# Kernel tuning notes

Hardware: AMD Instinct MI355X
Metric: run time of the kernel (lower is better)

The kernel has to match this reference:

```python
import jax, jax.numpy as jnp
import numpy as np

N_GRAPHS = 20000
N_NODES = 7          # nodes per NAS cell
HID = 256            # hidden_dim
N_OPS = 5
TAU = 1.0


def _glorot(key, shape):
    s = 1.0 / np.sqrt(shape[0])
    return jax.random.normal(key, shape, jnp.float32) * s


def setup_inputs() -> dict:
    key = jax.random.key(0)
    ks = jax.random.split(key, 12)
    N = N_GRAPHS * N_NODES
    # fully-connected DAG edges inside each graph (upper triangular, 21 per graph)
    sl, dl = np.triu_indices(N_NODES, k=1)
    offs = (np.arange(N_GRAPHS) * N_NODES)[:, None]
    src = (offs + sl[None, :]).reshape(-1)
    dst = (offs + dl[None, :]).reshape(-1)
    edge_index = jnp.asarray(np.stack([src, dst]), dtype=jnp.int32)  # [2, E]
    batch = jnp.asarray(np.repeat(np.arange(N_GRAPHS), N_NODES), dtype=jnp.int32)
    E = edge_index.shape[1]
    return {
        "x": jax.random.normal(ks[0], (N, HID), jnp.float32),
        "edge_index": edge_index,
        "batch": batch,
        "W1": _glorot(ks[1], (HID, HID)), "b1": jnp.zeros((HID,), jnp.float32),
        "W2": _glorot(ks[2], (HID, HID)), "b2": jnp.zeros((HID,), jnp.float32),
        "We": _glorot(ks[3], (2 * HID, 2)), "be": jnp.zeros((2,), jnp.float32),
        "Wm": _glorot(ks[4], (HID, N_OPS)), "bm": jnp.zeros((N_OPS,), jnp.float32),
        "g_edge": jax.random.gumbel(ks[5], (E, 2), jnp.float32),
        "g_op": jax.random.gumbel(ks[6], (N, N_OPS), jnp.float32),
    }


def gcn_conv(x, edge_index, W, b, edge_weight=None):
    """PyG-style GCNConv: add self-loops (weight 1), symmetric normalization."""
    N = x.shape[0]
    src, dst = edge_index[0], edge_index[1]
    E = src.shape[0]
    ew = jnp.ones((E,), x.dtype) if edge_weight is None else edge_weight
    loop = jnp.arange(N, dtype=src.dtype)
    src_a = jnp.concatenate([src, loop])
    dst_a = jnp.concatenate([dst, loop])
    ew_a = jnp.concatenate([ew, jnp.ones((N,), x.dtype)])
    deg = jax.ops.segment_sum(ew_a, dst_a, num_segments=N)
    dinv = jnp.where(deg > 0, jax.lax.rsqrt(jnp.maximum(deg, 1e-12)), 0.0)
    norm = dinv[src_a] * ew_a * dinv[dst_a]  # [E+N]
    h = x @ W  # [N, out]
    msg = norm[:, None] * h[src_a]
    return jax.ops.segment_sum(msg, dst_a, num_segments=N) + b


def gumbel_softmax(logits, g, tau, hard):
    y = jax.nn.softmax((logits + g) / tau, axis=-1)
    if hard:
        y_hard = jax.nn.one_hot(jnp.argmax(y, axis=-1), y.shape[-1], dtype=y.dtype)
        y = y_hard + y - jax.lax.stop_gradient(y)
    return y


def reference(x, edge_index, batch, W1, b1, W2, b2, We, be, Wm, bm, g_edge, g_op):
    # mu=2 GCN layers with ReLU
    h = jax.nn.relu(gcn_conv(x, edge_index, W1, b1))
    h = jax.nn.relu(gcn_conv(h, edge_index, W2, b2))
    # edge scorer: 2-way gumbel-softmax over (keep, drop) per edge
    src, dst = edge_index[0], edge_index[1]
    pair = jnp.concatenate([h[src], h[dst]], axis=-1)  # [E, 2*HID]
    edge_logits = pair @ We + be                       # [E, 2]
    edges_scores = gumbel_softmax(edge_logits, g_edge, TAU, hard=False)
    # sample_pre=False branch: average the two score channels as edge weight
    avg_scores = (edges_scores[:, 0] + edges_scores[:, 1]) / 2
    op_emb = gcn_conv(h, edge_index, Wm, bm, edge_weight=avg_scores)  # [N, N_OPS]
    # hard straight-through gumbel-softmax over operations
    op_indices = gumbel_softmax(op_emb, g_op, TAU, hard=True)
    return op_indices
```

## Files before the change

### kernel.cpp

```cpp
#include <hip/hip_runtime.h>
#include <math.h>

#define HID 256

typedef __attribute__((ext_vector_type(8))) short v8s;
typedef __attribute__((ext_vector_type(4))) float v4f;

__device__ __forceinline__ float d1c(int i){ return 1.0f/sqrtf((float)(i+1)); }
__device__ __forceinline__ float d2c(int i){ return 1.0f/sqrtf(1.0f+0.5f*(float)i); }

__device__ __forceinline__ unsigned short f2bf(float x){
    unsigned u = __float_as_uint(x);
    u += 0x7fffu + ((u>>16)&1u);
    return (unsigned short)(u>>16);
}
__device__ __forceinline__ float bf2f(unsigned short b){
    return __uint_as_float(((unsigned)b)<<16);
}

__device__ __forceinline__ void mixA1_4(float (&v)[7][4]) {
#pragma unroll
    for (int r = 6; r >= 0; --r) {
        float t[4] = {0, 0, 0, 0};
#pragma unroll
        for (int i = 0; i <= r; ++i) {
            const float c = d1c(i) * d1c(r);
#pragma unroll
            for (int j = 0; j < 4; ++j) t[j] = fmaf(c, v[i][j], t[j]);
        }
#pragma unroll
        for (int j = 0; j < 4; ++j) v[r][j] = t[j];
    }
}

__global__ void prep_w(const float* __restrict__ W1, const float* __restrict__ W2,
                       unsigned short* __restrict__ outw)
{
    const int tid = blockIdx.x*256 + threadIdx.x;
    if (tid >= 2*3*8*16*64) return;
    const int l  = tid & 63;
    const int c  = tid >> 6;
    const int nt = c & 15;
    const int k0 = (c>>4) & 7;
    const int s  = (c>>7) % 3;
    const int L  = c / (3*8*16);
    const float* W = L ? W2 : W1;
    const int n = nt*16 + (l & 15);
    unsigned short* o = outw + (size_t)tid*8;
#pragma unroll
    for (int e = 0; e < 8; ++e){
        const int k = k0*32 + (l>>4)*8 + e;
        float x = W[k*HID + n];
        unsigned short b0 = f2bf(x); float rr = x - bf2f(b0);
        unsigned short b1 = f2bf(rr); rr -= bf2f(b1);
        unsigned short b2 = f2bf(rr);
        o[e] = (s==0)? b0 : (s==1)? b1 : b2;
    }
}

__global__ __launch_bounds__(256, 2)
void nas_mfma(const float* __restrict__ X,
              const float* __restrict__ b1, const float* __restrict__ b2,
              const float* __restrict__ Wm, const float* __restrict__ bm,
              const float* __restrict__ g_op,
              const unsigned short* __restrict__ Bw,
              float* __restrict__ out)
{
    __shared__ __align__(16) char smem[49152 + 32768];
    char*  sb  = smem;
    float* bnc = (float*)(smem + 49152);

    const int t   = threadIdx.x;
    const int w   = t >> 6;
    const int l   = t & 63;
    const int l15 = l & 15;
    const int q   = l >> 4;
    const int g   = t >> 5;
    const int t31 = t & 31;
    const long node0 = (long)blockIdx.x * 56;

    auto writeSplits = [&](const float (&v)[7][4]){
        const int kl   = 4*t31;
        const int hs   = kl >> 3;
        const int sub8 = (kl & 7) * 2;
#pragma unroll
        for (int r = 0; r < 7; ++r){
            const int row  = g*7 + r;
            const int slot = hs ^ (row & 7);
            char* p = sb + row*256 + slot*16 + sub8;
            unsigned short h0[4], h1[4], h2[4];
#pragma unroll
            for (int j = 0; j < 4; ++j){
                float x = v[r][j];
                h0[j] = f2bf(x); float rr = x - bf2f(h0[j]);
                h1[j] = f2bf(rr); rr -= bf2f(h1[j]);
                h2[j] = f2bf(rr);
            }
            *(uint2*)(p)         = make_uint2((unsigned)h0[0]|((unsigned)h0[1]<<16),
                                              (unsigned)h0[2]|((unsigned)h0[3]<<16));
            *(uint2*)(p+16384)   = make_uint2((unsigned)h1[0]|((unsigned)h1[1]<<16),
                                              (unsigned)h1[2]|((unsigned)h1[3]<<16));
            *(uint2*)(p+32768)   = make_uint2((unsigned)h2[0]|((unsigned)h2[1]<<16),
                                              (unsigned)h2[2]|((unsigned)h2[3]<<16));
        }
    };

    auto gemm_half = [&](v4f (&ac)[4][4], const unsigned short* lbase, int h){
        const unsigned short* bbase = lbase + (size_t)w*512 + (size_t)l*8;
        v8s Bb[3][4];
        v8s A[3][4];
        auto loadB = [&](int gi, int buf){
            const int ks = gi / 3, s2 = gi % 3;
            const unsigned short* bp = bbase + (size_t)((s2*8 + h*4 + ks)*16)*512;
            Bb[buf][0] = *(const v8s*)(bp);
            Bb[buf][1] = *(const v8s*)(bp + 2048);
            Bb[buf][2] = *(const v8s*)(bp + 4096);
            Bb[buf][3] = *(const v8s*)(bp + 6144);
        };
        loadB(0, 0);
        loadB(1, 1);
#pragma unroll
        for (int gi = 0; gi < 12; ++gi){
            const int ks = gi / 3, s2 = gi % 3;
            if (s2 == 0){
                const int xorslot = ((ks*4 + q) ^ (l & 7)) << 4;
#pragma unroll
                for (int s = 0; s < 3; ++s)
#pragma unroll
                for (int mt = 0; mt < 4; ++mt)
                    A[s][mt] = *(const v8s*)(sb + s*16384 + (mt*16 + l15)*256 + xorslot);
            }
            if (gi + 2 < 12) loadB(gi + 2, (gi + 2) % 3);
            const int buf = gi % 3;
#pragma unroll
            for (int s1 = 0; s1 < 3; ++s1){
                if (s1 + s2 > 2) continue;
#pragma unroll
                for (int mt = 0; mt < 4; ++mt){
                    ac[mt][0] = __builtin_amdgcn_mfma_f32_16x16x32_bf16(A[s1][mt], Bb[buf][0], ac[mt][0],0,0,0);
                    ac[mt][1] = __builtin_amdgcn_mfma_f32_16x16x32_bf16(A[s1][mt], Bb[buf][1], ac[mt][1],0,0,0);
                    ac[mt][2] = __builtin_amdgcn_mfma_f32_16x16x32_bf16(A[s1][mt], Bb[buf][2], ac[mt][2],0,0,0);
                    ac[mt][3] = __builtin_amdgcn_mfma_f32_16x16x32_bf16(A[s1][mt], Bb[buf][3], ac[mt][3],0,0,0);
                }
            }
        }
    };

    auto bw2 = [&](const v4f (&ac)[4][4], int h){
#pragma unroll
        for (int pb = 0; pb < 2; ++pb){
            const int p  = 2*h + pb;
            const int lc = (w + 4*pb)*16 + l15;
#pragma unroll
            for (int mt = 0; mt < 4; ++mt){
                const int sw = ((q&1)<<4) ^ ((q>>1)<<2);
#pragma unroll
                for (int j = 0; j < 4; ++j){
                    const int row = mt*16 + q*4 + j;
                    bnc[row*128 + (lc ^ sw)] = ac[mt][p][j];
                }
            }
        }
    };
    auto br2 = [&](float (&v)[7][4]){
        const int lc = 4*t31;
#pragma unroll
        for (int r = 0; r < 7; ++r){
            const int row = g*7 + r;
            const int qq  = (row>>2)&3;
            const int sw  = ((qq&1)<<4) ^ ((qq>>1)<<2);
            float4 f = *(const float4*)(&bnc[row*128 + (lc ^ sw)]);
            v[r][0]=f.x; v[r][1]=f.y; v[r][2]=f.z; v[r][3]=f.w;
        }
    };
    auto biasRelu = [&](float (&v)[7][4], const float* bias, int h){
        float4 bb = *(const float4*)(bias + h*128 + 4*t31);
        const float bia[4] = {bb.x, bb.y, bb.z, bb.w};
#pragma unroll
        for (int r = 0; r < 7; ++r)
#pragma unroll
        for (int j = 0; j < 4; ++j)
            v[r][j] = fmaxf(v[r][j] + bia[j], 0.0f);
    };

    v4f acc[4][4];
#pragma unroll
    for (int mt=0;mt<4;++mt)
#pragma unroll
    for (int p=0;p<4;++p) acc[mt][p] = (v4f){0.f,0.f,0.f,0.f};

    float vh1[7][4];
    {
        float v0[7][4];
        const float* xp = X + (node0 + g*7)*HID + 4*t31;
#pragma unroll
        for (int r = 0; r < 7; ++r){
            float4 f0 = *(const float4*)(xp + (long)r*HID);
            float4 f1 = *(const float4*)(xp + (long)r*HID + 128);
            v0[r][0]=f0.x; v0[r][1]=f0.y; v0[r][2]=f0.z; v0[r][3]=f0.w;
            vh1[r][0]=f1.x; vh1[r][1]=f1.y; vh1[r][2]=f1.z; vh1[r][3]=f1.w;
        }
        mixA1_4(v0);
        mixA1_4(vh1);
        writeSplits(v0);
    }
    __syncthreads();
    gemm_half(acc, Bw, 0);
    __syncthreads();
    writeSplits(vh1);
    __syncthreads();
    gemm_half(acc, Bw, 1);

    v4f acc2[4][4];
#pragma unroll
    for (int mt=0;mt<4;++mt)
#pragma unroll
    for (int p=0;p<4;++p) acc2[mt][p] = (v4f){0.f,0.f,0.f,0.f};

    __syncthreads();
    bw2(acc, 0);
    __syncthreads();
    {
        float v[7][4];
        br2(v);
        biasRelu(v, b1, 0);
        mixA1_4(v);
        writeSplits(v);
    }
    __syncthreads();
    bw2(acc, 1);
    __syncthreads();
    br2(vh1);
    biasRelu(vh1, b1, 1);
    mixA1_4(vh1);
    gemm_half(acc2, Bw + 196608, 0);
    __syncthreads();
    writeSplits(vh1);
    __syncthreads();
    gemm_half(acc2, Bw + 196608, 1);

    float pm[7][5];
#pragma unroll
    for (int r=0;r<7;++r)
#pragma unroll
    for (int p=0;p<5;++p) pm[r][p] = 0.0f;

    auto stage_pm = [&](int h){
        float v[7][4];
        br2(v);
        biasRelu(v, b2, h);
        const int colg = h*128 + 4*t31;
#pragma unroll
        for (int j = 0; j < 4; ++j){
            const float* wr = Wm + (colg + j)*5;
            float w5[5];
#pragma unroll
            for (int p = 0; p < 5; ++p) w5[p] = wr[p];
#pragma unroll
            for (int r = 0; r < 7; ++r)
#pragma unroll
            for (int p = 0; p < 5; ++p)
                pm[r][p] = fmaf(v[r][j], w5[p], pm[r][p]);
        }
    };

    __syncthreads();
    bw2(acc2, 0);
    __syncthreads();
    stage_pm(0);
    __syncthreads();
    bw2(acc2, 1);
    __syncthreads();
    stage_pm(1);

#pragma unroll
    for (int m = 16; m >= 1; m >>= 1)
#pragma unroll
        for (int r = 0; r < 7; ++r)
#pragma unroll
            for (int p = 0; p < 5; ++p)
                pm[r][p] += __shfl_xor(pm[r][p], m, 64);

    if (t31 < 7){
        const int rr = t31;
        const long node = node0 + g*7 + rr;
        const float d2r = d2c(rr);
        float op[5];
#pragma unroll
        for (int p = 0; p < 5; ++p) op[p] = bm[p];
#pragma unroll
        for (int i = 0; i < 7; ++i){
            const float wgt = (i > rr) ? 0.0f
                            : (((i < rr) ? 0.5f : 1.0f) * d2c(i) * d2r);
#pragma unroll
            for (int p = 0; p < 5; ++p)
                op[p] = fmaf(wgt, pm[i][p], op[p]);
        }
        const float* gp = g_op + node*5;
        float best = op[0] + gp[0];
        int bi = 0;
#pragma unroll
        for (int p = 1; p < 5; ++p){
            float u = op[p] + gp[p];
            if (u > best) { best = u; bi = p; }
        }
        float* o = out + node*5;
#pragma unroll
        for (int p = 0; p < 5; ++p) o[p] = (p == bi) ? 1.0f : 0.0f;
    }
}

extern "C" void kernel_launch(void* const* d_in, const int* in_sizes, int n_in,
                              void* d_out, int out_size, void* d_ws, size_t ws_size,
                              hipStream_t stream)
{
    const float* X   = (const float*)d_in[0];
    const float* W1  = (const float*)d_in[3];
    const float* b1  = (const float*)d_in[4];
    const float* W2  = (const float*)d_in[5];
    const float* b2  = (const float*)d_in[6];
    const float* Wm  = (const float*)d_in[9];
    const float* bm  = (const float*)d_in[10];
    const float* gop = (const float*)d_in[12];
    float* out = (float*)d_out;

    unsigned short* wsplit = (unsigned short*)d_ws;

    prep_w<<<192, 256, 0, stream>>>(W1, W2, wsplit);

    const int N       = in_sizes[0] / HID;
    const int ngraph  = N / 7;
    const int nblocks = ngraph / 8;

    nas_mfma<<<nblocks, 256, 0, stream>>>(X, b1, b2, Wm, bm, gop, wsplit, out);
}
```

Baseline: 400.6 us.

## Split GEMM K into quarters with double-buffered LDS to overlap staging and MFMA

The K dimension of each layer's fused GEMM is now split into four 64-wide quarters instead of two halves. Two LDS buffers alternate, so writing the bf16 splits of the next quarter overlaps the MFMA of the current one. Shared memory drops from 80KB to 48KB, which could allow more resident blocks. The MFMA loops are wrapped in s_setprio raises. The cost is more barriers and narrower float2 LDS accesses, and register pressure rises because all four quarters of x are kept live at once.

Measured after the change: 403.9 us. Within noise of the previous version (+0.8%).

```diff
diff --git a/kernel.cpp b/kernel.cpp
--- a/kernel.cpp
+++ b/kernel.cpp
@@ -18,18 +18,17 @@
     return __uint_as_float(((unsigned)b)<<16);
 }
 
-__device__ __forceinline__ void mixA1_4(float (&v)[7][4]) {
+__device__ __forceinline__ void mixA1_2(float (&v)[7][2]) {
 #pragma unroll
     for (int r = 6; r >= 0; --r) {
-        float t[4] = {0, 0, 0, 0};
+        float t0 = 0.f, t1 = 0.f;
 #pragma unroll
         for (int i = 0; i <= r; ++i) {
             const float c = d1c(i) * d1c(r);
-#pragma unroll
-            for (int j = 0; j < 4; ++j) t[j] = fmaf(c, v[i][j], t[j]);
-        }
-#pragma unroll
-        for (int j = 0; j < 4; ++j) v[r][j] = t[j];
+            t0 = fmaf(c, v[i][0], t0);
+            t1 = fmaf(c, v[i][1], t1);
+        }
+        v[r][0] = t0; v[r][1] = t1;
     }
 }
 
@@ -66,9 +65,12 @@
               const unsigned short* __restrict__ Bw,
               float* __restrict__ out)
 {
-    __shared__ __align__(16) char smem[49152 + 32768];
-    char*  sb  = smem;
-    float* bnc = (float*)(smem + 49152);
+    __shared__ __align__(16) char smem[49152];
+    char*  Q0  = smem;
+    char*  Q1  = smem + 24576;
+    float* bq0 = (float*)smem;
+    float* bq1 = (float*)(smem + 24576);
+    float* bnc = (float*)smem;
 
     const int t   = threadIdx.x;
     const int w   = t >> 6;
@@ -79,39 +81,36 @@
     const int t31 = t & 31;
     const long node0 = (long)blockIdx.x * 56;
 
-    auto writeSplits = [&](const float (&v)[7][4]){
-        const int kl   = 4*t31;
-        const int hs   = kl >> 3;
-        const int sub8 = (kl & 7) * 2;
+    auto ws_q = [&](const float (&v)[7][2], char* qb){
+        const int slotbase = t31 >> 2;
+        const int byteoff  = (t31 & 3) * 4;
 #pragma unroll
         for (int r = 0; r < 7; ++r){
             const int row  = g*7 + r;
-            const int slot = hs ^ (row & 7);
-            char* p = sb + row*256 + slot*16 + sub8;
-            unsigned short h0[4], h1[4], h2[4];
-#pragma unroll
-            for (int j = 0; j < 4; ++j){
+            const int slot = slotbase ^ (row & 7);
+            char* p = qb + row*128 + slot*16 + byteoff;
+            unsigned h0[2], h1[2], h2[2];
+#pragma unroll
+            for (int j = 0; j < 2; ++j){
                 float x = v[r][j];
-                h0[j] = f2bf(x); float rr = x - bf2f(h0[j]);
-                h1[j] = f2bf(rr); rr -= bf2f(h1[j]);
-                h2[j] = f2bf(rr);
+                unsigned short a = f2bf(x); float rr = x - bf2f(a);
+                unsigned short b = f2bf(rr); rr -= bf2f(b);
+                unsigned short c = f2bf(rr);
+                h0[j] = a; h1[j] = b; h2[j] = c;
             }
-            *(uint2*)(p)         = make_uint2((unsigned)h0[0]|((unsigned)h0[1]<<16),
-                                              (unsigned)h0[2]|((unsigned)h0[3]<<16));
-            *(uint2*)(p+16384)   = make_uint2((unsigned)h1[0]|((unsigned)h1[1]<<16),
-                                              (unsigned)h1[2]|((unsigned)h1[3]<<16));
-            *(uint2*)(p+32768)   = make_uint2((unsigned)h2[0]|((unsigned)h2[1]<<16),
-                                              (unsigned)h2[2]|((unsigned)h2[3]<<16));
-        }
-    };
-
-    auto gemm_half = [&](v4f (&ac)[4][4], const unsigned short* lbase, int h){
+            *(unsigned*)(p)         = h0[0] | (h0[1] << 16);
+            *(unsigned*)(p + 8192)  = h1[0] | (h1[1] << 16);
+            *(unsigned*)(p + 16384) = h2[0] | (h2[1] << 16);
+        }
+    };
+
+    auto gemm_q = [&](v4f (&ac)[4][4], const unsigned short* lbase, int qi,
+                      const char* qb){
         const unsigned short* bbase = lbase + (size_t)w*512 + (size_t)l*8;
         v8s Bb[3][4];
-        v8s A[3][4];
         auto loadB = [&](int gi, int buf){
-            const int ks = gi / 3, s2 = gi % 3;
-            const unsigned short* bp = bbase + (size_t)((s2*8 + h*4 + ks)*16)*512;
+            const int ksl = gi/3, s2 = gi%3;
+            const unsigned short* bp = bbase + (size_t)((s2*8 + qi*2 + ksl)*16)*512;
             Bb[buf][0] = *(const v8s*)(bp);
             Bb[buf][1] = *(const v8s*)(bp + 2048);
             Bb[buf][2] = *(const v8s*)(bp + 4096);
@@ -119,19 +118,21 @@
         };
         loadB(0, 0);
         loadB(1, 1);
-#pragma unroll
-        for (int gi = 0; gi < 12; ++gi){
-            const int ks = gi / 3, s2 = gi % 3;
+        v8s A[3][4];
+#pragma unroll
+        for (int gi = 0; gi < 6; ++gi){
+            const int ksl = gi/3, s2 = gi%3;
             if (s2 == 0){
-                const int xorslot = ((ks*4 + q) ^ (l & 7)) << 4;
+                const int xorslot = ((ksl*4 + q) ^ (l15 & 7)) << 4;
 #pragma unroll
                 for (int s = 0; s < 3; ++s)
 #pragma unroll
                 for (int mt = 0; mt < 4; ++mt)
-                    A[s][mt] = *(const v8s*)(sb + s*16384 + (mt*16 + l15)*256 + xorslot);
+                    A[s][mt] = *(const v8s*)(qb + s*8192 + (mt*16 + l15)*128 + xorslot);
             }
-            if (gi + 2 < 12) loadB(gi + 2, (gi + 2) % 3);
+            if (gi + 2 < 6) loadB(gi + 2, (gi + 2) % 3);
             const int buf = gi % 3;
+            __builtin_amdgcn_s_setprio(1);
 #pragma unroll
             for (int s1 = 0; s1 < 3; ++s1){
                 if (s1 + s2 > 2) continue;
@@ -143,26 +144,117 @@
                     ac[mt][3] = __builtin_amdgcn_mfma_f32_16x16x32_bf16(A[s1][mt], Bb[buf][3], ac[mt][3],0,0,0);
                 }
             }
-        }
-    };
+            __builtin_amdgcn_s_setprio(0);
+        }
+    };
+
+    auto bw_q = [&](const v4f (&ac)[4][4], int p, float* bq){
+        const int cc = (w*16 + l15) ^ (q << 4);
+#pragma unroll
+        for (int mt = 0; mt < 4; ++mt)
+#pragma unroll
+        for (int j = 0; j < 4; ++j)
+            bq[(mt*16 + q*4 + j)*64 + cc] = ac[mt][p][j];
+    };
+    auto rd_q = [&](float (&v)[7][2], const float* bq){
+#pragma unroll
+        for (int r = 0; r < 7; ++r){
+            const int row = g*7 + r;
+            const int sw  = ((row >> 2) & 3) << 4;
+            float2 f = *(const float2*)(&bq[row*64 + ((2*t31) ^ sw)]);
+            v[r][0] = f.x; v[r][1] = f.y;
+        }
+    };
+    auto brm = [&](float (&v)[7][2], const float* bias, int p){
+        float2 bb = *(const float2*)(bias + p*64 + 2*t31);
+#pragma unroll
+        for (int r = 0; r < 7; ++r){
+            v[r][0] = fmaxf(v[r][0] + bb.x, 0.0f);
+            v[r][1] = fmaxf(v[r][1] + bb.y, 0.0f);
+        }
+        mixA1_2(v);
+    };
+
+    v4f acc[4][4];
+#pragma unroll
+    for (int mt=0;mt<4;++mt)
+#pragma unroll
+    for (int p=0;p<4;++p) acc[mt][p] = (v4f){0.f,0.f,0.f,0.f};
+
+    float xq[4][7][2];
+    {
+        const float* xp = X + (node0 + g*7)*HID + 2*t31;
+#pragma unroll
+        for (int r = 0; r < 7; ++r)
+#pragma unroll
+        for (int qq = 0; qq < 4; ++qq){
+            float2 f = *(const float2*)(xp + (long)r*HID + qq*64);
+            xq[qq][r][0] = f.x; xq[qq][r][1] = f.y;
+        }
+#pragma unroll
+        for (int qq = 0; qq < 4; ++qq) mixA1_2(xq[qq]);
+    }
+
+    ws_q(xq[0], Q0);
+    __syncthreads();
+    ws_q(xq[1], Q1); gemm_q(acc, Bw, 0, Q0);
+    __syncthreads();
+    ws_q(xq[2], Q0); gemm_q(acc, Bw, 1, Q1);
+    __syncthreads();
+    ws_q(xq[3], Q1); gemm_q(acc, Bw, 2, Q0);
+    __syncthreads();
+    gemm_q(acc, Bw, 3, Q1); bw_q(acc, 0, bq0);
+    __syncthreads();
+
+    v4f acc2[4][4];
+#pragma unroll
+    for (int mt=0;mt<4;++mt)
+#pragma unroll
+    for (int p=0;p<4;++p) acc2[mt][p] = (v4f){0.f,0.f,0.f,0.f};
+    const unsigned short* Bw2 = Bw + 196608;
+
+    float v0[7][2], v1[7][2];
+    rd_q(v0, bq0); bw_q(acc, 1, bq1);
+    __syncthreads();
+    brm(v0, b1, 0); ws_q(v0, Q0); rd_q(v1, bq1);
+    __syncthreads();
+    brm(v1, b1, 1); ws_q(v1, Q1); gemm_q(acc2, Bw2, 0, Q0);
+    __syncthreads();
+    bw_q(acc, 2, bq0); gemm_q(acc2, Bw2, 1, Q1);
+    __syncthreads();
+    rd_q(v0, bq0); bw_q(acc, 3, bq1);
+    __syncthreads();
+    brm(v0, b1, 2); ws_q(v0, Q0); rd_q(v1, bq1);
+    __syncthreads();
+    brm(v1, b1, 3); ws_q(v1, Q1); gemm_q(acc2, Bw2, 2, Q0);
+    __syncthreads();
+    gemm_q(acc2, Bw2, 3, Q1);
+    __syncthreads();
 
     auto bw2 = [&](const v4f (&ac)[4][4], int h){
 #pragma unroll
         for (int pb = 0; pb < 2; ++pb){
             const int p  = 2*h + pb;
             const int lc = (w + 4*pb)*16 + l15;
-#pragma unroll
-            for (int mt = 0; mt < 4; ++mt){
-                const int sw = ((q&1)<<4) ^ ((q>>1)<<2);
-#pragma unroll
-                for (int j = 0; j < 4; ++j){
-                    const int row = mt*16 + q*4 + j;
-                    bnc[row*128 + (lc ^ sw)] = ac[mt][p][j];
-                }
+            const int sw = ((q&1)<<4) ^ ((q>>1)<<2);
+#pragma unroll
+            for (int mt = 0; mt < 4; ++mt)
+#pragma unroll
+            for (int j = 0; j < 4; ++j){
+                const int row = mt*16 + q*4 + j;
+                bnc[row*128 + (lc ^ sw)] = ac[mt][p][j];
             }
         }
     };
-    auto br2 = [&](float (&v)[7][4]){
+
+    float pm[7][5];
+#pragma unroll
+    for (int r=0;r<7;++r)
+#pragma unroll
+    for (int p=0;p<5;++p) pm[r][p] = 0.0f;
+
+    auto stage_pm = [&](int h){
+        float v[7][4];
         const int lc = 4*t31;
 #pragma unroll
         for (int r = 0; r < 7; ++r){
@@ -172,83 +264,13 @@
             float4 f = *(const float4*)(&bnc[row*128 + (lc ^ sw)]);
             v[r][0]=f.x; v[r][1]=f.y; v[r][2]=f.z; v[r][3]=f.w;
         }
-    };
-    auto biasRelu = [&](float (&v)[7][4], const float* bias, int h){
-        float4 bb = *(const float4*)(bias + h*128 + 4*t31);
+        float4 bb = *(const float4*)(b2 + h*128 + 4*t31);
         const float bia[4] = {bb.x, bb.y, bb.z, bb.w};
 #pragma unroll
         for (int r = 0; r < 7; ++r)
 #pragma unroll
         for (int j = 0; j < 4; ++j)
             v[r][j] = fmaxf(v[r][j] + bia[j], 0.0f);
-    };
-
-    v4f acc[4][4];
-#pragma unroll
-    for (int mt=0;mt<4;++mt)
-#pragma unroll
-    for (int p=0;p<4;++p) acc[mt][p] = (v4f){0.f,0.f,0.f,0.f};
-
-    float vh1[7][4];
-    {
-        float v0[7][4];
-        const float* xp = X + (node0 + g*7)*HID + 4*t31;
-#pragma unroll
-        for (int r = 0; r < 7; ++r){
-            float4 f0 = *(const float4*)(xp + (long)r*HID);
-            float4 f1 = *(const float4*)(xp + (long)r*HID + 128);
-            v0[r][0]=f0.x; v0[r][1]=f0.y; v0[r][2]=f0.z; v0[r][3]=f0.w;
-            vh1[r][0]=f1.x; vh1[r][1]=f1.y; vh1[r][2]=f1.z; vh1[r][3]=f1.w;
-        }
-        mixA1_4(v0);
-        mixA1_4(vh1);
-        writeSplits(v0);
-    }
-    __syncthreads();
-    gemm_half(acc, Bw, 0);
-    __syncthreads();
-    writeSplits(vh1);
-    __syncthreads();
-    gemm_half(acc, Bw, 1);
-
-    v4f acc2[4][4];
-#pragma unroll
-    for (int mt=0;mt<4;++mt)
-#pragma unroll
-    for (int p=0;p<4;++p) acc2[mt][p] = (v4f){0.f,0.f,0.f,0.f};
-
-    __syncthreads();
-    bw2(acc, 0);
-    __syncthreads();
-    {
-        float v[7][4];
-        br2(v);
-        biasRelu(v, b1, 0);
-        mixA1_4(v);
-        writeSplits(v);
-    }
-    __syncthreads();
-    bw2(acc, 1);
-    __syncthreads();
-    br2(vh1);
-    biasRelu(vh1, b1, 1);
-    mixA1_4(vh1);
-    gemm_half(acc2, Bw + 196608, 0);
-    __syncthreads();
-    writeSplits(vh1);
-    __syncthreads();
-    gemm_half(acc2, Bw + 196608, 1);
-
-    float pm[7][5];
-#pragma unroll
-    for (int r=0;r<7;++r)
-#pragma unroll
-    for (int p=0;p<5;++p) pm[r][p] = 0.0f;
-
-    auto stage_pm = [&](int h){
-        float v[7][4];
-        br2(v);
-        biasRelu(v, b2, h);
         const int colg = h*128 + 4*t31;
 #pragma unroll
         for (int j = 0; j < 4; ++j){
@@ -264,7 +286,6 @@
         }
     };
 
-    __syncthreads();
     bw2(acc2, 0);
     __syncthreads();
     stage_pm(0);
```
